# Optimization experiments

Measured on AMD Instinct MI355X. Metric: run time of the kernel, lower is better.

## Reference

```python
import jax, jax.numpy as jnp
import numpy as np

B, S, D, H = 2, 2048, 1024, 16
HD = D // H  # head_dim = 64
EPS = 1e-12


def setup_inputs() -> dict:
    key = jax.random.key(0)
    ks = jax.random.split(key, 12)
    s = 0.02
    return {
        "hidden_states": jax.random.normal(ks[0], (B, S, D), jnp.float32),
        "attention_mask": jnp.zeros((B, 1, 1, S), jnp.float32),
        "alibi_bias": jax.random.normal(ks[1], (1, H, S, S), jnp.float32) * 0.1,
        "Wq": jax.random.normal(ks[2], (D, D), jnp.float32) * s,
        "bq": jnp.zeros((D,), jnp.float32),
        "Wk": jax.random.normal(ks[3], (D, D), jnp.float32) * s,
        "bk": jnp.zeros((D,), jnp.float32),
        "Wv": jax.random.normal(ks[4], (D, D), jnp.float32) * s,
        "bv": jnp.zeros((D,), jnp.float32),
        "Wo": jax.random.normal(ks[5], (D, D), jnp.float32) * s,
        "bo": jnp.zeros((D,), jnp.float32),
        "ln_gamma": jnp.ones((D,), jnp.float32),
        "ln_beta": jnp.zeros((D,), jnp.float32),
    }


def _split_heads(x):
    # [B, S, D] -> [B, H, S, HD]
    return x.reshape(B, S, H, HD).transpose(0, 2, 1, 3)


def reference(hidden_states, attention_mask, alibi_bias,
              Wq, bq, Wk, bk, Wv, bv, Wo, bo, ln_gamma, ln_beta):
    q = _split_heads(hidden_states @ Wq + bq)
    k = _split_heads(hidden_states @ Wk + bk)
    v = _split_heads(hidden_states @ Wv + bv)

    scale = HD ** -0.5
    # combined additive mask: [B,1,1,S] + [1,H,S,S] -> broadcast [B,H,S,S]
    combined_mask = attention_mask + alibi_bias
    scores = jnp.einsum('bhqd,bhkd->bhqk', q, k) * scale + combined_mask
    probs = jax.nn.softmax(scores, axis=-1)
    attn = jnp.einsum('bhqk,bhkd->bhqd', probs, v)  # [B,H,S,HD]
    attn = attn.transpose(0, 2, 1, 3).reshape(B, S, D)

    out = attn @ Wo + bo
    x = hidden_states + out  # post-norm residual
    mu = jnp.mean(x, axis=-1, keepdims=True)
    var = jnp.mean(jnp.square(x - mu), axis=-1, keepdims=True)
    return (x - mu) * jax.lax.rsqrt(var + EPS) * ln_gamma + ln_beta
```

## Files before the change

### kernel.cpp

```cpp
#include <hip/hip_runtime.h>

#define Bb 2
#define Ss 2048
#define Dd 1024
#define Hh 16
#define HD 64
#define Mm (Bb*Ss)
#define KVB 64

typedef __bf16 bf16;
typedef __bf16 bf16x8 __attribute__((ext_vector_type(8)));
typedef float f32x4 __attribute__((ext_vector_type(4)));

#define GL(gp, lp) __builtin_amdgcn_global_load_lds( \
        (const __attribute__((address_space(1))) unsigned int*)(gp), \
        (__attribute__((address_space(3))) unsigned int*)(lp), 16, 0, 0)

__global__ void cvt_f32_bf16(const float* __restrict__ in, bf16* __restrict__ out, int n4) {
    int i = blockIdx.x * blockDim.x + threadIdx.x;
    if (i < n4) {
        float4 v = *(const float4*)(in + i * 4);
        out[i*4+0] = (bf16)v.x; out[i*4+1] = (bf16)v.y;
        out[i*4+2] = (bf16)v.z; out[i*4+3] = (bf16)v.w;
    }
}

__global__ void wtrans(const float* __restrict__ W0, const float* __restrict__ W1,
                       const float* __restrict__ W2, const float* __restrict__ W3,
                       bf16* __restrict__ O0, bf16* __restrict__ O1,
                       bf16* __restrict__ O2, bf16* __restrict__ O3) {
    const float* W = (blockIdx.z == 0) ? W0 : (blockIdx.z == 1) ? W1 : (blockIdx.z == 2) ? W2 : W3;
    bf16* O = (blockIdx.z == 0) ? O0 : (blockIdx.z == 1) ? O1 : (blockIdx.z == 2) ? O2 : O3;
    __shared__ bf16 t[64][65];
    int k0 = blockIdx.x * 64, n0 = blockIdx.y * 64;
    for (int c = threadIdx.x; c < 4096; c += 256) {
        int r = c >> 6, cc = c & 63;
        t[r][cc] = (bf16)W[(k0 + r) * Dd + n0 + cc];
    }
    __syncthreads();
    for (int c = threadIdx.x; c < 4096; c += 256) {
        int r = c >> 6, cc = c & 63;
        O[(n0 + r) * Dd + k0 + cc] = t[cc][r];
    }
}

__global__ void vtrans(const bf16* __restrict__ in, bf16* __restrict__ out) {
    __shared__ bf16 t[64][72];
    int s0 = blockIdx.x * 64, bh = blockIdx.y;
    int tid = threadIdx.x;
    int r = tid >> 3, c = (tid & 7) * 8;
    const bf16* ib = in + ((size_t)bh * Ss + s0) * HD;
    bf16x8 v0 = *(const bf16x8*)(&ib[(size_t)r * HD + c]);
    bf16x8 v1 = *(const bf16x8*)(&ib[(size_t)(r + 32) * HD + c]);
    *(bf16x8*)(&t[r][c]) = v0;
    *(bf16x8*)(&t[r + 32][c]) = v1;
    __syncthreads();
    int d0 = tid >> 3, d1 = d0 + 32, sc2 = (tid & 7) * 8;
    bf16x8 o0, o1;
#pragma unroll
    for (int e = 0; e < 8; e++) { o0[e] = t[sc2 + e][d0]; o1[e] = t[sc2 + e][d1]; }
    *(bf16x8*)(&out[((size_t)(bh * HD + d0)) * Ss + s0 + sc2]) = o0;
    *(bf16x8*)(&out[((size_t)(bh * HD + d1)) * Ss + s0 + sc2]) = o1;
}

template<int BM>
__global__ __launch_bounds__(256, (BM == 64) ? 4 : 3)
void gemm_bt(const bf16* __restrict__ A, const bf16* __restrict__ Bt,
             const float* __restrict__ b0, const float* __restrict__ b1, const float* __restrict__ b2,
             bf16* __restrict__ o0, bf16* __restrict__ o1, bf16* __restrict__ o2, int mode) {
    const int K = 1024;
    constexpr int MI = BM / 32;
    __shared__ __align__(16) bf16 As[2][BM * 32];
    __shared__ __align__(16) bf16 Bs[2][128 * 32];
    int tid = threadIdx.x;
    int wave = tid >> 6, lane = tid & 63;
    int lane15 = lane & 15, quad = lane >> 4;
    int wm = (wave >> 1) * (BM / 2), wn = (wave & 1) * 64;
    int m0 = blockIdx.x * BM, n0 = blockIdx.y * 128;
    int lrow = lane >> 2, lcol = (lane & 3) * 8;
    const bf16* Ag = &A[(size_t)(m0 + wave * 16 + lrow) * K + lcol];
    const bf16* Bg = &Bt[(size_t)(n0 + wave * 16 + lrow) * K + lcol];

    f32x4 acc[MI][4] = {};

#define STAGE(buf, kt) do { \
        bf16* Asw = &As[buf][wave * 16 * 32]; \
        bf16* Bsw = &Bs[buf][wave * 16 * 32]; \
        GL(Ag + (kt), Asw); \
        if constexpr (BM == 128) GL(Ag + 64 * K + (kt), Asw + 64 * 32); \
        GL(Bg + (kt), Bsw); \
        GL(Bg + 64 * K + (kt), Bsw + 64 * 32); \
    } while (0)

    STAGE(0, 0);
    __syncthreads();
    int cur = 0;
    for (int kt = 0; kt < K; kt += 32) {
        if (kt + 32 < K) STAGE(cur ^ 1, kt + 32);
        bf16x8 af[MI], bfr[4];
#pragma unroll
        for (int i = 0; i < MI; i++) af[i] = *(const bf16x8*)(&As[cur][(wm + i * 16 + lane15) * 32 + quad * 8]);
#pragma unroll
        for (int j = 0; j < 4; j++) bfr[j] = *(const bf16x8*)(&Bs[cur][(wn + j * 16 + lane15) * 32 + quad * 8]);
#pragma unroll
        for (int i = 0; i < MI; i++)
#pragma unroll
            for (int j = 0; j < 4; j++)
                acc[i][j] = __builtin_amdgcn_mfma_f32_16x16x32_bf16(af[i], bfr[j], acc[i][j], 0, 0, 0);
        __syncthreads();
        cur ^= 1;
    }
#undef STAGE

#pragma unroll
    for (int i = 0; i < MI; i++) {
        int mbase = m0 + wm + i * 16 + quad * 4;
#pragma unroll
        for (int j = 0; j < 4; j++) {
            int n = n0 + wn + j * 16 + lane15;
            if (mode == 0) {
                float bv = b0[n];
#pragma unroll
                for (int r = 0; r < 4; r++)
                    o0[(size_t)(mbase + r) * 1024 + n] = (bf16)(acc[i][j][r] + bv);
            } else {
                int which = n >> 10, nn = n & 1023;
                const float* bp = (which == 0) ? b0 : (which == 1) ? b1 : b2;
                bf16* op = (which == 0) ? o0 : (which == 1) ? o1 : o2;
                float bv = bp[nn];
                int hh = nn >> 6, hd = nn & 63;
#pragma unroll
                for (int r = 0; r < 4; r++) {
                    int m = mbase + r;
                    int bb = m >> 11, s = m & 2047;
                    op[(((size_t)(bb * Hh + hh) * Ss + s) * HD) + hd] = (bf16)(acc[i][j][r] + bv);
                }
            }
        }
    }
}

__global__ __launch_bounds__(256, 2)
void attn_kernel(const bf16* __restrict__ Q, const bf16* __restrict__ Kk, const bf16* __restrict__ Vt,
                 const float* __restrict__ alibi, const float* __restrict__ mask,
                 bf16* __restrict__ outattn) {
    int hwid = blockIdx.x;
    int b = (hwid >> 3) & 1;
    int pid = ((hwid >> 4) << 3) | (hwid & 7);
    int qt = pid & 31, h = pid >> 5;

    __shared__ __align__(16) bf16 Ks[2][64 * 64];
    __shared__ __align__(16) bf16 Vts[2][64 * 64];
    __shared__ __align__(16) float Als[2][64 * 64];
    __shared__ __align__(16) bf16 QPs[64 * 64];
    __shared__ __align__(16) float Ms[2048];

    int tid = threadIdx.x, wave = tid >> 6, lane = tid & 63;
    int lane15 = lane & 15, quad = lane >> 4;

    const bf16* Qbase = Q + ((size_t)(b * Hh + h) * Ss + qt * 64) * HD;
    const bf16* Kbase = Kk + (size_t)(b * Hh + h) * Ss * HD;
    const bf16* Vtbase = Vt + (size_t)(b * Hh + h) * HD * Ss;
    const float* Abase = alibi + ((size_t)h * Ss + qt * 64) * Ss;
    const float* Mbase = mask + (size_t)b * Ss;

    int r8_0 = wave * 16 + (lane >> 3);
    int r8_1 = r8_0 + 8;
    int c8_0 = ((lane & 7) * 8) ^ ((r8_0 & 7) * 8);
    int c8_1 = ((lane & 7) * 8) ^ ((r8_1 & 7) * 8);
    int ra[4], ca[4];
#pragma unroll
    for (int c = 0; c < 4; c++) {
        ra[c] = wave * 16 + c * 4 + (lane >> 4);
        ca[c] = ((lane & 15) * 4) ^ (((ra[c] >> 2) & 1) * 16);
    }
    const bf16* Kg0 = Kbase + (size_t)r8_0 * HD + c8_0;
    const bf16* Kg1 = Kbase + (size_t)r8_1 * HD + c8_1;
    const bf16* Vg0 = Vtbase + (size_t)r8_0 * Ss + c8_0;
    const bf16* Vg1 = Vtbase + (size_t)r8_1 * Ss + c8_1;
    const float* Ag0 = Abase + (size_t)ra[0] * Ss + ca[0];
    const float* Ag1 = Abase + (size_t)ra[1] * Ss + ca[1];
    const float* Ag2 = Abase + (size_t)ra[2] * Ss + ca[2];
    const float* Ag3 = Abase + (size_t)ra[3] * Ss + ca[3];

    GL(Qbase + (size_t)r8_0 * HD + c8_0, &QPs[wave * 1024]);
    GL(Qbase + (size_t)r8_1 * HD + c8_1, &QPs[wave * 1024 + 512]);
    GL(Mbase + wave * 512 + lane * 4,        &Ms[wave * 512]);
    GL(Mbase + wave * 512 + 256 + lane * 4,  &Ms[wave * 512 + 256]);
    GL(Kg0, &Ks[0][wave * 1024]);
    GL(Kg1, &Ks[0][wave * 1024 + 512]);
    GL(Vg0, &Vts[0][wave * 1024]);
    GL(Vg1, &Vts[0][wave * 1024 + 512]);
    GL(Ag0, &Als[0][wave * 1024]);
    GL(Ag1, &Als[0][wave * 1024 + 256]);
    GL(Ag2, &Als[0][wave * 1024 + 512]);
    GL(Ag3, &Als[0][wave * 1024 + 768]);
    __syncthreads();

    int qrow = wave * 16 + lane15;
    bf16x8 qf0 = *(const bf16x8*)(&QPs[qrow * 64 + ((quad * 8) ^ ((qrow & 7) * 8))]);
    bf16x8 qf1 = *(const bf16x8*)(&QPs[qrow * 64 + ((32 + quad * 8) ^ ((qrow & 7) * 8))]);

    float m_i[4], l_i[4];
    f32x4 O[4] = {};
#pragma unroll
    for (int r = 0; r < 4; r++) { m_i[r] = -1e30f; l_i[r] = 0.f; }

    const float scale = 0.125f;

    int cur = 0;
    for (int kt = 0; kt < Ss; kt += KVB) {
        int nxt = cur ^ 1;
        if (kt + KVB < Ss) {
            int kn = kt + KVB;
            GL(Kg0 + (size_t)kn * HD, &Ks[nxt][wave * 1024]);
            GL(Kg1 + (size_t)kn * HD, &Ks[nxt][wave * 1024 + 512]);
            GL(Vg0 + kn, &Vts[nxt][wave * 1024]);
            GL(Vg1 + kn, &Vts[nxt][wave * 1024 + 512]);
            GL(Ag0 + kn, &Als[nxt][wave * 1024]);
            GL(Ag1 + kn, &Als[nxt][wave * 1024 + 256]);
            GL(Ag2 + kn, &Als[nxt][wave * 1024 + 512]);
            GL(Ag3 + kn, &Als[nxt][wave * 1024 + 768]);
        }

        f32x4 sc[4];
        f32x4 z = {0.f, 0.f, 0.f, 0.f};
#pragma unroll
        for (int j = 0; j < 4; j++) {
            int krow = j * 16 + lane15;
            bf16x8 kf0 = *(const bf16x8*)(&Ks[cur][krow * 64 + ((quad * 8) ^ ((krow & 7) * 8))]);
            bf16x8 kf1 = *(const bf16x8*)(&Ks[cur][krow * 64 + ((32 + quad * 8) ^ ((krow & 7) * 8))]);
            f32x4 s = __builtin_amdgcn_mfma_f32_16x16x32_bf16(qf0, kf0, z, 0, 0, 0);
            s = __builtin_amdgcn_mfma_f32_16x16x32_bf16(qf1, kf1, s, 0, 0, 0);
            sc[j] = s;
        }
#pragma unroll
        for (int j = 0; j < 4; j++) {
            int col = j * 16 + lane15;
            float mk = Ms[kt + col];
#pragma unroll
            for (int r = 0; r < 4; r++) {
                int arow = wave * 16 + quad * 4 + r;
                float al = Als[cur][arow * 64 + (col ^ (((arow >> 2) & 1) * 16))];
                sc[j][r] = sc[j][r] * scale + al + mk;
            }
        }
        float alpha[4];
#pragma unroll
        for (int r = 0; r < 4; r++) {
            float v = fmaxf(fmaxf(sc[0][r], sc[1][r]), fmaxf(sc[2][r], sc[3][r]));
#pragma unroll
            for (int d = 1; d < 16; d <<= 1) v = fmaxf(v, __shfl_xor(v, d, 64));
            float mnew = fmaxf(m_i[r], v);
            alpha[r] = __expf(m_i[r] - mnew);
            m_i[r] = mnew;
        }
        float rs[4] = {0.f, 0.f, 0.f, 0.f};
#pragma unroll
        for (int j = 0; j < 4; j++)
#pragma unroll
            for (int r = 0; r < 4; r++) {
                float p = __expf(sc[j][r] - m_i[r]);
                sc[j][r] = p;
                rs[r] += p;
            }
#pragma unroll
        for (int r = 0; r < 4; r++) {
            float v = rs[r];
#pragma unroll
            for (int d = 1; d < 16; d <<= 1) v += __shfl_xor(v, d, 64);
            l_i[r] = l_i[r] * alpha[r] + v;
        }
#pragma unroll
        for (int j = 0; j < 4; j++)
#pragma unroll
            for (int r = 0; r < 4; r++) {
                int row = wave * 16 + quad * 4 + r;
                QPs[row * 64 + ((j * 16 + lane15) ^ ((row & 7) * 8))] = (bf16)sc[j][r];
            }
        asm volatile("s_waitcnt lgkmcnt(0)" ::: "memory");
        int prow = wave * 16 + lane15;
        bf16x8 pf0 = *(const bf16x8*)(&QPs[prow * 64 + ((quad * 8) ^ ((prow & 7) * 8))]);
        bf16x8 pf1 = *(const bf16x8*)(&QPs[prow * 64 + ((32 + quad * 8) ^ ((prow & 7) * 8))]);
#pragma unroll
        for (int jd = 0; jd < 4; jd++) {
            int vrow = jd * 16 + lane15;
#pragma unroll
            for (int r = 0; r < 4; r++) O[jd][r] *= alpha[r];
            bf16x8 vf0 = *(const bf16x8*)(&Vts[cur][vrow * 64 + ((quad * 8) ^ ((vrow & 7) * 8))]);
            bf16x8 vf1 = *(const bf16x8*)(&Vts[cur][vrow * 64 + ((32 + quad * 8) ^ ((vrow & 7) * 8))]);
            O[jd] = __builtin_amdgcn_mfma_f32_16x16x32_bf16(pf0, vf0, O[jd], 0, 0, 0);
            O[jd] = __builtin_amdgcn_mfma_f32_16x16x32_bf16(pf1, vf1, O[jd], 0, 0, 0);
        }
        __syncthreads();
        cur = nxt;
    }

#pragma unroll
    for (int jd = 0; jd < 4; jd++) {
        int d = jd * 16 + lane15;
#pragma unroll
        for (int r = 0; r < 4; r++) {
            int qg = qt * 64 + wave * 16 + quad * 4 + r;
            float v = O[jd][r] / l_i[r];
            outattn[(((size_t)b * Ss + qg) * Hh + h) * HD + d] = (bf16)v;
        }
    }
}

__global__ void ln_kernel(const float* __restrict__ hidden, const bf16* __restrict__ Y,
                          const float* __restrict__ gamma, const float* __restrict__ beta,
                          float* __restrict__ out) {
    int row = blockIdx.x;
    int tid = threadIdx.x, wave = tid >> 6, lane = tid & 63;
    float x[4];
    float s = 0.f, q = 0.f;
#pragma unroll
    for (int e = 0; e < 4; e++) {
        int col = e * 256 + tid;
        x[e] = hidden[(size_t)row * Dd + col] + (float)Y[(size_t)row * Dd + col];
        s += x[e];
        q += x[e] * x[e];
    }
#pragma unroll
    for (int d = 1; d < 64; d <<= 1) { s += __shfl_xor(s, d, 64); q += __shfl_xor(q, d, 64); }
    __shared__ float sm[4], sq[4];
    if (lane == 0) { sm[wave] = s; sq[wave] = q; }
    __syncthreads();
    float tot = sm[0] + sm[1] + sm[2] + sm[3];
    float totq = sq[0] + sq[1] + sq[2] + sq[3];
    float mu = tot * (1.f / 1024.f);
    float var = totq * (1.f / 1024.f) - mu * mu;
    float rstd = rsqrtf(var + 1e-12f);
#pragma unroll
    for (int e = 0; e < 4; e++) {
        int col = e * 256 + tid;
        out[(size_t)row * Dd + col] = (x[e] - mu) * rstd * gamma[col] + beta[col];
    }
}

extern "C" void kernel_launch(void* const* d_in, const int* in_sizes, int n_in,
                              void* d_out, int out_size, void* d_ws, size_t ws_size,
                              hipStream_t stream) {
    const float* hidden = (const float*)d_in[0];
    const float* amask  = (const float*)d_in[1];
    const float* alibi  = (const float*)d_in[2];
    const float* Wq = (const float*)d_in[3];
    const float* bq = (const float*)d_in[4];
    const float* Wk = (const float*)d_in[5];
    const float* bk = (const float*)d_in[6];
    const float* Wv = (const float*)d_in[7];
    const float* bv = (const float*)d_in[8];
    const float* Wo = (const float*)d_in[9];
    const float* bo = (const float*)d_in[10];
    const float* ln_g = (const float*)d_in[11];
    const float* ln_b = (const float*)d_in[12];
    float* out = (float*)d_out;

    char* w = (char*)d_ws;
    bf16* Xb   = (bf16*)(w);
    bf16* WqT  = (bf16*)(w + 8388608);
    bf16* WkT  = (bf16*)(w + 10485760);
    bf16* WvT  = (bf16*)(w + 12582912);
    bf16* WoT  = (bf16*)(w + 14680064);
    bf16* Qw   = (bf16*)(w + 16777216);
    bf16* Kw   = (bf16*)(w + 25165824);
    bf16* Vw   = (bf16*)(w + 33554432);
    bf16* Attn = (bf16*)(w + 41943040);
    bf16* Yw   = (bf16*)(w + 50331648);
    bf16* Vtw  = Xb;

    cvt_f32_bf16<<<4096, 256, 0, stream>>>(hidden, Xb, Mm * Dd / 4);
    wtrans<<<dim3(16, 16, 4), 256, 0, stream>>>(Wq, Wk, Wv, Wo, WqT, WkT, WvT, WoT);

    gemm_bt<128><<<dim3(32, 24), 256, 0, stream>>>(Xb, WqT, bq, bk, bv, Qw, Kw, Vw, 1);

    vtrans<<<dim3(32, 32), 256, 0, stream>>>(Vw, Vtw);

    attn_kernel<<<1024, 256, 0, stream>>>(Qw, Kw, Vtw, alibi, amask, Attn);

    gemm_bt<64><<<dim3(64, 8), 256, 0, stream>>>(Attn, WoT, bo, nullptr, nullptr, Yw, nullptr, nullptr, 0);

    ln_kernel<<<4096, 256, 0, stream>>>(hidden, Yw, ln_g, ln_b, out);
}
```

Baseline: 567.7 us.

## Load alibi bias and mask directly to registers, raise attention occupancy, vectorize LayerNorm

The attention kernel no longer stages the fp32 alibi tile and the mask in double-buffered shared memory. Each lane now reads its alibi and mask values straight from global memory into registers at the top of every KV iteration. This frees about 40KB of LDS, and launch bounds are raised to 4 blocks per CU to allow more occupancy. The LayerNorm kernel switches to float4/bf16x4 vector loads and stores. The trade-off is that alibi loads become strided, non-prefetched per-lane global reads (16-lane contiguous segments) issued just before they are used, which may expose latency and add register pressure.

```diff
diff --git a/kernel.cpp b/kernel.cpp
--- a/kernel.cpp
+++ b/kernel.cpp
@@ -10,6 +10,7 @@
 
 typedef __bf16 bf16;
 typedef __bf16 bf16x8 __attribute__((ext_vector_type(8)));
+typedef __bf16 bf16x4 __attribute__((ext_vector_type(4)));
 typedef float f32x4 __attribute__((ext_vector_type(4)));
 
 #define GL(gp, lp) __builtin_amdgcn_global_load_lds( \
@@ -140,7 +141,7 @@
     }
 }
 
-__global__ __launch_bounds__(256, 2)
+__global__ __launch_bounds__(256, 4)
 void attn_kernel(const bf16* __restrict__ Q, const bf16* __restrict__ Kk, const bf16* __restrict__ Vt,
                  const float* __restrict__ alibi, const float* __restrict__ mask,
                  bf16* __restrict__ outattn) {
@@ -151,9 +152,7 @@
 
     __shared__ __align__(16) bf16 Ks[2][64 * 64];
     __shared__ __align__(16) bf16 Vts[2][64 * 64];
-    __shared__ __align__(16) float Als[2][64 * 64];
     __shared__ __align__(16) bf16 QPs[64 * 64];
-    __shared__ __align__(16) float Ms[2048];
 
     int tid = threadIdx.x, wave = tid >> 6, lane = tid & 63;
     int lane15 = lane & 15, quad = lane >> 4;
@@ -161,40 +160,24 @@
     const bf16* Qbase = Q + ((size_t)(b * Hh + h) * Ss + qt * 64) * HD;
     const bf16* Kbase = Kk + (size_t)(b * Hh + h) * Ss * HD;
     const bf16* Vtbase = Vt + (size_t)(b * Hh + h) * HD * Ss;
-    const float* Abase = alibi + ((size_t)h * Ss + qt * 64) * Ss;
+    const float* alibi_q = alibi + ((size_t)h * Ss + qt * 64 + wave * 16 + quad * 4) * Ss;
     const float* Mbase = mask + (size_t)b * Ss;
 
     int r8_0 = wave * 16 + (lane >> 3);
     int r8_1 = r8_0 + 8;
     int c8_0 = ((lane & 7) * 8) ^ ((r8_0 & 7) * 8);
     int c8_1 = ((lane & 7) * 8) ^ ((r8_1 & 7) * 8);
-    int ra[4], ca[4];
-#pragma unroll
-    for (int c = 0; c < 4; c++) {
-        ra[c] = wave * 16 + c * 4 + (lane >> 4);
-        ca[c] = ((lane & 15) * 4) ^ (((ra[c] >> 2) & 1) * 16);
-    }
     const bf16* Kg0 = Kbase + (size_t)r8_0 * HD + c8_0;
     const bf16* Kg1 = Kbase + (size_t)r8_1 * HD + c8_1;
     const bf16* Vg0 = Vtbase + (size_t)r8_0 * Ss + c8_0;
     const bf16* Vg1 = Vtbase + (size_t)r8_1 * Ss + c8_1;
-    const float* Ag0 = Abase + (size_t)ra[0] * Ss + ca[0];
-    const float* Ag1 = Abase + (size_t)ra[1] * Ss + ca[1];
-    const float* Ag2 = Abase + (size_t)ra[2] * Ss + ca[2];
-    const float* Ag3 = Abase + (size_t)ra[3] * Ss + ca[3];
 
     GL(Qbase + (size_t)r8_0 * HD + c8_0, &QPs[wave * 1024]);
     GL(Qbase + (size_t)r8_1 * HD + c8_1, &QPs[wave * 1024 + 512]);
-    GL(Mbase + wave * 512 + lane * 4,        &Ms[wave * 512]);
-    GL(Mbase + wave * 512 + 256 + lane * 4,  &Ms[wave * 512 + 256]);
     GL(Kg0, &Ks[0][wave * 1024]);
     GL(Kg1, &Ks[0][wave * 1024 + 512]);
     GL(Vg0, &Vts[0][wave * 1024]);
     GL(Vg1, &Vts[0][wave * 1024 + 512]);
-    GL(Ag0, &Als[0][wave * 1024]);
-    GL(Ag1, &Als[0][wave * 1024 + 256]);
-    GL(Ag2, &Als[0][wave * 1024 + 512]);
-    GL(Ag3, &Als[0][wave * 1024 + 768]);
     __syncthreads();
 
     int qrow = wave * 16 + lane15;
@@ -211,16 +194,20 @@
     int cur = 0;
     for (int kt = 0; kt < Ss; kt += KVB) {
         int nxt = cur ^ 1;
+        float al[4][4], mk[4];
+#pragma unroll
+        for (int j = 0; j < 4; j++) {
+#pragma unroll
+            for (int r = 0; r < 4; r++)
+                al[j][r] = alibi_q[(size_t)r * Ss + kt + j * 16 + lane15];
+            mk[j] = Mbase[kt + j * 16 + lane15];
+        }
         if (kt + KVB < Ss) {
             int kn = kt + KVB;
             GL(Kg0 + (size_t)kn * HD, &Ks[nxt][wave * 1024]);
             GL(Kg1 + (size_t)kn * HD, &Ks[nxt][wave * 1024 + 512]);
             GL(Vg0 + kn, &Vts[nxt][wave * 1024]);
             GL(Vg1 + kn, &Vts[nxt][wave * 1024 + 512]);
-            GL(Ag0 + kn, &Als[nxt][wave * 1024]);
-            GL(Ag1 + kn, &Als[nxt][wave * 1024 + 256]);
-            GL(Ag2 + kn, &Als[nxt][wave * 1024 + 512]);
-            GL(Ag3 + kn, &Als[nxt][wave * 1024 + 768]);
         }
 
         f32x4 sc[4];
@@ -235,16 +222,10 @@
             sc[j] = s;
         }
 #pragma unroll
-        for (int j = 0; j < 4; j++) {
-            int col = j * 16 + lane15;
-            float mk = Ms[kt + col];
-#pragma unroll
-            for (int r = 0; r < 4; r++) {
-                int arow = wave * 16 + quad * 4 + r;
-                float al = Als[cur][arow * 64 + (col ^ (((arow >> 2) & 1) * 16))];
-                sc[j][r] = sc[j][r] * scale + al + mk;
-            }
-        }
+        for (int j = 0; j < 4; j++)
+#pragma unroll
+            for (int r = 0; r < 4; r++)
+                sc[j][r] = sc[j][r] * scale + al[j][r] + mk[j];
         float alpha[4];
 #pragma unroll
         for (int r = 0; r < 4; r++) {
@@ -313,15 +294,13 @@
                           float* __restrict__ out) {
     int row = blockIdx.x;
     int tid = threadIdx.x, wave = tid >> 6, lane = tid & 63;
-    float x[4];
+    float4 hv = *(const float4*)(&hidden[(size_t)row * Dd + tid * 4]);
+    bf16x4 yv = *(const bf16x4*)(&Y[(size_t)row * Dd + tid * 4]);
+    float x[4] = {hv.x + (float)yv[0], hv.y + (float)yv[1],
+                  hv.z + (float)yv[2], hv.w + (float)yv[3]};
     float s = 0.f, q = 0.f;
 #pragma unroll
-    for (int e = 0; e < 4; e++) {
-        int col = e * 256 + tid;
-        x[e] = hidden[(size_t)row * Dd + col] + (float)Y[(size_t)row * Dd + col];
-        s += x[e];
-        q += x[e] * x[e];
-    }
+    for (int e = 0; e < 4; e++) { s += x[e]; q += x[e] * x[e]; }
 #pragma unroll
     for (int d = 1; d < 64; d <<= 1) { s += __shfl_xor(s, d, 64); q += __shfl_xor(q, d, 64); }
     __shared__ float sm[4], sq[4];
@@ -332,11 +311,14 @@
     float mu = tot * (1.f / 1024.f);
     float var = totq * (1.f / 1024.f) - mu * mu;
     float rstd = rsqrtf(var + 1e-12f);
-#pragma unroll
-    for (int e = 0; e < 4; e++) {
-        int col = e * 256 + tid;
-        out[(size_t)row * Dd + col] = (x[e] - mu) * rstd * gamma[col] + beta[col];
-    }
+    float4 gv = *(const float4*)(&gamma[tid * 4]);
+    float4 bv = *(const float4*)(&beta[tid * 4]);
+    float4 ov;
+    ov.x = (x[0] - mu) * rstd * gv.x + bv.x;
+    ov.y = (x[1] - mu) * rstd * gv.y + bv.y;
+    ov.z = (x[2] - mu) * rstd * gv.z + bv.z;
+    ov.w = (x[3] - mu) * rstd * gv.w + bv.w;
+    *(float4*)(&out[(size_t)row * Dd + tid * 4]) = ov;
 }
 
 extern "C" void kernel_launch(void* const* d_in, const int* in_sizes, int n_in,
```

Measured after the change: 535.9 us. 5.6% less time.
